# Kernel optimization log

Measured on AMD Instinct MI355X. Metric: run time of the kernel, lower is better.

Reference implementation:

```python
import jax, jax.numpy as jnp
import numpy as np

V, D, H, E, C, K = 16000, 1024, 1024, 8, 16, 2  # vocab, embed, expert hidden, n_experts, classes, top_k
B, S = 64, 512
GATE_H = 256


def setup_inputs() -> dict:
    key = jax.random.key(0)
    ks = jax.random.split(key, 11)
    s = lambda i, shape: jax.random.normal(ks[i], shape, jnp.float32) * 0.02
    return dict(
        x=jax.random.randint(ks[0], (B, S), 0, V),
        emb=s(1, (V, D)),                      # shared gating embedding
        gate_w1=s(2, (D, GATE_H)), gate_b1=jnp.zeros((GATE_H,), jnp.float32),
        gate_w2=s(3, (GATE_H, E)), gate_b2=jnp.zeros((E,), jnp.float32),
        exp_emb=s(4, (E, V, D)),               # per-expert embedding tables
        exp_w1=s(5, (E, D, H)), exp_b1=jnp.zeros((E, H), jnp.float32),
        exp_w2=s(6, (E, H, C)), exp_b2=jnp.zeros((E, C), jnp.float32),
    )


def reference(x, emb, gate_w1, gate_b1, gate_w2, gate_b2,
              exp_emb, exp_w1, exp_b1, exp_w2, exp_b2):
    # --- gating: embed, mean-pool over seq, 2-layer MLP, softmax, top-k ---
    pooled = emb[x].mean(axis=1)                                   # [B,D]
    logits = jax.nn.relu(pooled @ gate_w1 + gate_b1) @ gate_w2 + gate_b2  # [B,E]
    probs = jax.nn.softmax(logits, axis=-1)
    rw, idx = jax.lax.top_k(probs, K)                              # [B,K]
    rw = rw / rw.sum(axis=-1, keepdims=True)                       # renormalize

    # --- dispatch: gather each sample's assigned expert params (no per-sample loop) ---
    out = jnp.zeros((x.shape[0], C), jnp.float32)
    for k in range(K):  # tiny fixed loop over top_k
        e = idx[:, k]                                              # [B]
        tok = exp_emb[e[:, None], x]                               # [B,S,D]
        h = jax.nn.relu(jnp.einsum('bsd,bdh->bsh', tok, exp_w1[e]) + exp_b1[e][:, None, :])  # [B,S,H]
        p = h.mean(axis=1)                                         # [B,H]
        eo = jnp.einsum('bh,bhc->bc', p, exp_w2[e]) + exp_b2[e]    # [B,C]
        out = out + rw[:, k:k + 1] * eo
    return out
```

## Files before the change

### kernel.cpp

```cpp
#include <hip/hip_runtime.h>
#include <hip/hip_bf16.h>

#define V_   16000
#define D_   1024
#define H_   1024
#define E_   8
#define C_   16
#define B_   64
#define S_   512
#define GH_  256
#define NPAIR 128

typedef short  bf16x8 __attribute__((ext_vector_type(8)));
typedef ushort u16x8  __attribute__((ext_vector_type(8)));
typedef float  f32x4  __attribute__((ext_vector_type(4)));

static __device__ __forceinline__ ushort f2bf(float f) {
  union { float f; unsigned u; } un; un.f = f;
  unsigned u = un.u;
  return (ushort)((u + 0x7FFFu + ((u >> 16) & 1u)) >> 16);
}

static __device__ __forceinline__ unsigned pk2(float lo, float hi) {
  __hip_bfloat162 h = __float22bfloat162_rn(make_float2(lo, hi));
  unsigned r; __builtin_memcpy(&r, &h, sizeof(r)); return r;
}

__global__ void prep_kernel(const float* __restrict__ w1, ushort* __restrict__ w1t,
                            const int* __restrict__ x, const float* __restrict__ emb,
                            float* __restrict__ partial) {
  __shared__ float tile[64][65];
  const int id = blockIdx.x;
  if (id < 2048) {
    const int e = id >> 8, rem = id & 255;
    const int dtile = rem & 15, htile = rem >> 4;
    const int d0 = dtile * 64, h0 = htile * 64;
    const float* src = w1 + (size_t)e * D_ * H_;
    for (int i = threadIdx.x; i < 64 * 64; i += 256) {
      int r = i >> 6, c = i & 63;
      tile[r][c] = src[(size_t)(d0 + r) * H_ + h0 + c];
    }
    __syncthreads();
    for (int i = threadIdx.x; i < 512; i += 256) {
      int chunk = i >> 6, lane = i & 63;
      int kkl = chunk >> 2, htl = chunk & 3;
      int l15 = lane & 15, l16 = lane >> 4;
      u16x8 v;
      #pragma unroll
      for (int j = 0; j < 8; ++j)
        v[j] = f2bf(tile[kkl * 32 + l16 * 8 + j][htl * 16 + l15]);
      size_t off = ((size_t)((e * 32 + dtile * 2 + kkl) * 64 + htile * 4 + htl)) * 512 + lane * 8;
      *reinterpret_cast<u16x8*>(w1t + off) = v;
    }
  } else {
    const int pid = id - 2048;
    const int b = pid >> 3, sb = pid & 7, t = threadIdx.x;
    const int* xr = x + b * S_ + sb * 64;
    float4 acc = make_float4(0.f, 0.f, 0.f, 0.f);
    #pragma unroll 4
    for (int s = 0; s < 64; ++s) {
      const float4* row = reinterpret_cast<const float4*>(emb + (size_t)xr[s] * D_);
      float4 v = row[t];
      acc.x += v.x; acc.y += v.y; acc.z += v.z; acc.w += v.w;
    }
    reinterpret_cast<float4*>(partial + ((size_t)b * 8 + sb) * D_)[t] = acc;
  }
}

__global__ void gate_kernel(const float* __restrict__ partial,
                            const float* __restrict__ gw1, const float* __restrict__ gb1,
                            const float* __restrict__ gw2, const float* __restrict__ gb2,
                            int* __restrict__ ridx, float* __restrict__ rwgt) {
  const int b = blockIdx.x, j = threadIdx.x;
  __shared__ float pl[D_];
  __shared__ float hid[GH_];
  __shared__ float logits[E_];
  for (int d = j; d < D_; d += 256) {
    float s = 0.f;
    #pragma unroll
    for (int sb = 0; sb < 8; ++sb) s += partial[((size_t)b * 8 + sb) * D_ + d];
    pl[d] = s * (1.f / (float)S_);
  }
  __syncthreads();
  float acc = gb1[j];
  for (int d = 0; d < D_; ++d) acc += pl[d] * gw1[d * GH_ + j];
  hid[j] = fmaxf(acc, 0.f);
  __syncthreads();
  if (j < E_) {
    float l = gb2[j];
    for (int i = 0; i < GH_; ++i) l += hid[i] * gw2[i * E_ + j];
    logits[j] = l;
  }
  __syncthreads();
  if (j == 0) {
    int i0 = 0; float v0 = logits[0];
    for (int i = 1; i < E_; ++i) if (logits[i] > v0) { v0 = logits[i]; i0 = i; }
    int i1 = -1; float v1 = -3.0e38f;
    for (int i = 0; i < E_; ++i) {
      if (i == i0) continue;
      if (logits[i] > v1) { v1 = logits[i]; i1 = i; }
    }
    float r1 = expf(v1 - v0);
    float norm = 1.f + r1;
    ridx[b * 2 + 0] = i0;         ridx[b * 2 + 1] = i1;
    rwgt[b * 2 + 0] = 1.f / norm; rwgt[b * 2 + 1] = r1 / norm;
  }
}

__global__ void sort_pairs_kernel(const int* __restrict__ ridx, int* __restrict__ order) {
  __shared__ int se[NPAIR];
  const int t = threadIdx.x;
  se[t] = ridx[t];
  __syncthreads();
  const int e = se[t];
  int rank = 0;
  for (int j = 0; j < NPAIR; ++j) {
    const int ej = se[j];
    rank += (ej < e || (ej == e && j < t)) ? 1 : 0;
  }
  order[rank] = t;
}

__global__ __launch_bounds__(1024) void expert_kernel(
    const int* __restrict__ x, const float* __restrict__ exp_emb,
    const ushort* __restrict__ w1t, const float* __restrict__ exp_b1,
    const int* __restrict__ ridx, const int* __restrict__ order,
    float* __restrict__ p_part) {
  const int id     = blockIdx.x;
  const int xcd    = id & 7;
  const int within = id >> 3;
  const int slot   = xcd * 128 + within;
  const int pr     = order[slot >> 3];
  const int sblk   = slot & 7;
  const int b      = pr >> 1;
  const int tid    = threadIdx.x;

  __shared__ __align__(16) ushort lB[64 * 1024];

  const int e = ridx[pr];

  const int grow = tid >> 4, kq4 = (tid & 15) * 4;
  const int tok  = x[b * S_ + sblk * 64 + grow];
  const float* gptr = exp_emb + ((size_t)e * V_ + tok) * D_ + kq4;
  const int swz  = (grow & 7) << 3;
  const int gdst = grow * 1024 + (((kq4 & ~7) ^ swz) + (kq4 & 7));

  const int wid = tid >> 6, lane = tid & 63;
  const int l15 = lane & 15, l16 = lane >> 4;
  const int sw  = (l15 & 7) << 3;

  const ushort* aLane = w1t + (size_t)e * (32 * 64 * 512)
                        + ((size_t)wid * 4) * 512 + (size_t)lane * 8;
  #define LOADA(kk_, i_) \
    (*reinterpret_cast<const bf16x8*>(aLane + ((size_t)((kk_) * 64 + (i_))) * 512))

  f32x4 acc[4][4];
  #pragma unroll
  for (int i = 0; i < 4; ++i)
    #pragma unroll
    for (int j = 0; j < 4; ++j) acc[i][j] = (f32x4){0.f, 0.f, 0.f, 0.f};

  f32x4 stP[2];
  stP[0] = __builtin_nontemporal_load(reinterpret_cast<const f32x4*>(gptr));
  {
    uint2 w;
    w.x = pk2(stP[0][0], stP[0][1]); w.y = pk2(stP[0][2], stP[0][3]);
    *reinterpret_cast<uint2*>(&lB[gdst]) = w;
  }
  stP[1] = __builtin_nontemporal_load(reinterpret_cast<const f32x4*>(gptr + 64));
  __syncthreads();

  #pragma unroll
  for (int s = 0; s < 16; ++s) {
    const int cur = s & 1;
    if (s + 2 < 16) {
      stP[cur] = __builtin_nontemporal_load(
          reinterpret_cast<const f32x4*>(gptr + (s + 2) * 64));
    }
    #pragma unroll
    for (int ks = 0; ks < 2; ++ks) {
      const int kk = s * 2 + ks;
      const int colk = s * 64 + (((ks << 5) | (l16 << 3)) ^ sw);
      bf16x8 bfr[4], af[4];
      #pragma unroll
      for (int j = 0; j < 4; ++j)
        bfr[j] = *reinterpret_cast<const bf16x8*>(&lB[(j * 16 + l15) * 1024 + colk]);
      #pragma unroll
      for (int i = 0; i < 4; ++i) af[i] = LOADA(kk, i);
      #pragma unroll
      for (int i = 0; i < 4; ++i)
        #pragma unroll
        for (int j = 0; j < 4; ++j)
          acc[i][j] = __builtin_amdgcn_mfma_f32_16x16x32_bf16(af[i], bfr[j], acc[i][j], 0, 0, 0);
    }
    if (s + 1 < 16) {
      uint2 w;
      w.x = pk2(stP[cur ^ 1][0], stP[cur ^ 1][1]);
      w.y = pk2(stP[cur ^ 1][2], stP[cur ^ 1][3]);
      *reinterpret_cast<uint2*>(&lB[gdst + (s + 1) * 64]) = w;
    }
    __syncthreads();
  }
  #undef LOADA

  float* outRow = p_part + (size_t)(sblk * NPAIR + pr) * H_;
  const float* biasE = exp_b1 + e * H_;
  #pragma unroll
  for (int i = 0; i < 4; ++i) {
    #pragma unroll
    for (int r = 0; r < 4; ++r) {
      const int h = wid * 64 + i * 16 + l16 * 4 + r;
      const float bias = biasE[h];
      float v = 0.f;
      #pragma unroll
      for (int j = 0; j < 4; ++j) v += fmaxf(acc[i][j][r] + bias, 0.f);
      #pragma unroll
      for (int m = 1; m < 16; m <<= 1) v += __shfl_xor(v, m);
      if (l15 == 0) outRow[h] = v;
    }
  }
}

__global__ void finalize_kernel(const float* __restrict__ p_part,
                                const int* __restrict__ ridx, const float* __restrict__ rwgt,
                                const float* __restrict__ w2, const float* __restrict__ b2,
                                float* __restrict__ out) {
  const int b = blockIdx.x, t = threadIdx.x;
  const int c = t & 15, g = t >> 4;
  __shared__ float red[16][17];
  float res = 0.f;
  for (int kk = 0; kk < 2; ++kk) {
    const int pr = b * 2 + kk;
    const int e = ridx[pr];
    const float w = rwgt[pr];
    float dot = 0.f;
    for (int h = g; h < H_; h += 16) {
      float pm = 0.f;
      #pragma unroll
      for (int sb = 0; sb < 8; ++sb) pm += p_part[(size_t)(sb * NPAIR + pr) * H_ + h];
      dot += pm * w2[((size_t)e * H_ + h) * C_ + c];
    }
    red[g][c] = dot;
    __syncthreads();
    if (g == 0) {
      float s = 0.f;
      #pragma unroll
      for (int i = 0; i < 16; ++i) s += red[i][c];
      res += w * (s * (1.f / (float)S_) + b2[e * C_ + c]);
    }
    __syncthreads();
  }
  if (g == 0) out[b * C_ + c] = res;
}

extern "C" void kernel_launch(void* const* d_in, const int* in_sizes, int n_in,
                              void* d_out, int out_size, void* d_ws, size_t ws_size,
                              hipStream_t stream) {
  const int*   x    = (const int*)  d_in[0];
  const float* emb  = (const float*)d_in[1];
  const float* gw1  = (const float*)d_in[2];
  const float* gb1  = (const float*)d_in[3];
  const float* gw2  = (const float*)d_in[4];
  const float* gb2  = (const float*)d_in[5];
  const float* eemb = (const float*)d_in[6];
  const float* ew1  = (const float*)d_in[7];
  const float* eb1  = (const float*)d_in[8];
  const float* ew2  = (const float*)d_in[9];
  const float* eb2  = (const float*)d_in[10];
  float* out = (float*)d_out;

  char* ws = (char*)d_ws;
  const size_t OFF_W1T   = 0;
  const size_t OFF_PART  = (size_t)16 << 20;
  const size_t OFF_RIDX  = OFF_PART + ((size_t)2 << 20);
  const size_t OFF_RWGT  = OFF_RIDX + 1024;
  const size_t OFF_ORDER = OFF_RWGT + 1024;
  const size_t OFF_PPART = OFF_ORDER + 1024;

  ushort* w1t    = (ushort*)(ws + OFF_W1T);
  float*  part   = (float*) (ws + OFF_PART);
  int*    ridx   = (int*)   (ws + OFF_RIDX);
  float*  rwgt   = (float*) (ws + OFF_RWGT);
  int*    order  = (int*)   (ws + OFF_ORDER);
  float*  ppart  = (float*) (ws + OFF_PPART);

  prep_kernel<<<dim3(2560), 256, 0, stream>>>(ew1, w1t, x, emb, part);
  gate_kernel<<<dim3(B_), 256, 0, stream>>>(part, gw1, gb1, gw2, gb2, ridx, rwgt);
  sort_pairs_kernel<<<dim3(1), 128, 0, stream>>>(ridx, order);
  expert_kernel<<<dim3(1024), 1024, 0, stream>>>(x, eemb, w1t, eb1, ridx, order, ppart);
  finalize_kernel<<<dim3(B_), 256, 0, stream>>>(ppart, ridx, rwgt, ew2, eb2, out);
}
```

Baseline: 256.7 us.

## Retile expert GEMM to 128-token by 512-hidden blocks with double-buffered LDS

Each expert block now covers 128 tokens and half of the hidden dimension instead of 64 tokens and all of it. Each wave computes an 8x2 MFMA tile, so one A-fragment global load is reused across two B fragments. LDS shrinks from a full 64x1024 token tile to two 128x64 ping-pong buffers, so the gathered embeddings are staged per k-step instead of kept whole. This is meant to cut LDS footprint and per-block W1 traffic, at the cost of more partial sums (16 instead of 8) for finalize to reduce. Launch bounds now request 4 blocks per CU.

```diff
diff --git a/kernel.cpp b/kernel.cpp
--- a/kernel.cpp
+++ b/kernel.cpp
@@ -24,6 +24,13 @@
 static __device__ __forceinline__ unsigned pk2(float lo, float hi) {
   __hip_bfloat162 h = __float22bfloat162_rn(make_float2(lo, hi));
   unsigned r; __builtin_memcpy(&r, &h, sizeof(r)); return r;
+}
+
+static __device__ __forceinline__ uint4 cvt8(f32x4 a, f32x4 b) {
+  uint4 w;
+  w.x = pk2(a[0], a[1]); w.y = pk2(a[2], a[3]);
+  w.z = pk2(b[0], b[1]); w.w = pk2(b[2], b[3]);
+  return w;
 }
 
 __global__ void prep_kernel(const float* __restrict__ w1, ushort* __restrict__ w1t,
@@ -121,7 +128,7 @@
   order[rank] = t;
 }
 
-__global__ __launch_bounds__(1024) void expert_kernel(
+__global__ __launch_bounds__(1024, 4) void expert_kernel(
     const int* __restrict__ x, const float* __restrict__ exp_emb,
     const ushort* __restrict__ w1t, const float* __restrict__ exp_b1,
     const int* __restrict__ ridx, const int* __restrict__ order,
@@ -130,93 +137,95 @@
   const int xcd    = id & 7;
   const int within = id >> 3;
   const int slot   = xcd * 128 + within;
-  const int pr     = order[slot >> 3];
-  const int sblk   = slot & 7;
+  const int ss     = slot >> 3;
+  const int sb4    = (slot >> 1) & 3;
+  const int hb     = slot & 1;
+  const int pr     = order[ss];
   const int b      = pr >> 1;
   const int tid    = threadIdx.x;
 
-  __shared__ __align__(16) ushort lB[64 * 1024];
+  __shared__ __align__(16) ushort lB[2][8192];
 
   const int e = ridx[pr];
 
-  const int grow = tid >> 4, kq4 = (tid & 15) * 4;
-  const int tok  = x[b * S_ + sblk * 64 + grow];
-  const float* gptr = exp_emb + ((size_t)e * V_ + tok) * D_ + kq4;
-  const int swz  = (grow & 7) << 3;
-  const int gdst = grow * 1024 + (((kq4 & ~7) ^ swz) + (kq4 & 7));
+  const int grow = tid >> 3, gkq = (tid & 7) * 8;
+  const int tok  = x[b * S_ + sb4 * 128 + grow];
+  const float* gptr = exp_emb + ((size_t)e * V_ + tok) * D_ + gkq;
+  const int bwidx = grow * 64 + (gkq ^ ((grow & 7) << 3));
 
   const int wid = tid >> 6, lane = tid & 63;
   const int l15 = lane & 15, l16 = lane >> 4;
-  const int sw  = (l15 & 7) << 3;
+  const int ws = wid & 3, wh = wid >> 2;
+  const int sw = (l15 & 7) << 3;
 
   const ushort* aLane = w1t + (size_t)e * (32 * 64 * 512)
-                        + ((size_t)wid * 4) * 512 + (size_t)lane * 8;
+                        + ((size_t)(hb * 32 + wh * 8)) * 512 + (size_t)lane * 8;
   #define LOADA(kk_, i_) \
     (*reinterpret_cast<const bf16x8*>(aLane + ((size_t)((kk_) * 64 + (i_))) * 512))
 
-  f32x4 acc[4][4];
+  f32x4 acc[8][2];
   #pragma unroll
-  for (int i = 0; i < 4; ++i)
+  for (int i = 0; i < 8; ++i)
     #pragma unroll
-    for (int j = 0; j < 4; ++j) acc[i][j] = (f32x4){0.f, 0.f, 0.f, 0.f};
-
-  f32x4 stP[2];
-  stP[0] = __builtin_nontemporal_load(reinterpret_cast<const f32x4*>(gptr));
-  {
-    uint2 w;
-    w.x = pk2(stP[0][0], stP[0][1]); w.y = pk2(stP[0][2], stP[0][3]);
-    *reinterpret_cast<uint2*>(&lB[gdst]) = w;
-  }
-  stP[1] = __builtin_nontemporal_load(reinterpret_cast<const f32x4*>(gptr + 64));
+    for (int j = 0; j < 2; ++j) acc[i][j] = (f32x4){0.f, 0.f, 0.f, 0.f};
+
+  f32x4 stP[2][2];
+  stP[0][0] = __builtin_nontemporal_load(reinterpret_cast<const f32x4*>(gptr));
+  stP[0][1] = __builtin_nontemporal_load(reinterpret_cast<const f32x4*>(gptr + 4));
+  *reinterpret_cast<uint4*>(&lB[0][bwidx]) = cvt8(stP[0][0], stP[0][1]);
+  stP[1][0] = __builtin_nontemporal_load(reinterpret_cast<const f32x4*>(gptr + 64));
+  stP[1][1] = __builtin_nontemporal_load(reinterpret_cast<const f32x4*>(gptr + 68));
   __syncthreads();
 
   #pragma unroll
   for (int s = 0; s < 16; ++s) {
     const int cur = s & 1;
     if (s + 2 < 16) {
-      stP[cur] = __builtin_nontemporal_load(
+      stP[cur][0] = __builtin_nontemporal_load(
           reinterpret_cast<const f32x4*>(gptr + (s + 2) * 64));
+      stP[cur][1] = __builtin_nontemporal_load(
+          reinterpret_cast<const f32x4*>(gptr + (s + 2) * 64 + 4));
     }
     #pragma unroll
     for (int ks = 0; ks < 2; ++ks) {
       const int kk = s * 2 + ks;
-      const int colk = s * 64 + (((ks << 5) | (l16 << 3)) ^ sw);
-      bf16x8 bfr[4], af[4];
-      #pragma unroll
-      for (int j = 0; j < 4; ++j)
-        bfr[j] = *reinterpret_cast<const bf16x8*>(&lB[(j * 16 + l15) * 1024 + colk]);
-      #pragma unroll
-      for (int i = 0; i < 4; ++i) af[i] = LOADA(kk, i);
-      #pragma unroll
-      for (int i = 0; i < 4; ++i)
+      const int colk = ((ks << 5) | (l16 << 3)) ^ sw;
+      bf16x8 bfr[2];
+      #pragma unroll
+      for (int j = 0; j < 2; ++j) {
+        const int row = ws * 32 + j * 16 + l15;
+        bfr[j] = *reinterpret_cast<const bf16x8*>(
+            &lB[cur][row * 64 + (((ks << 5) | (l16 << 3)) ^ ((row & 7) << 3))]);
+      }
+      #pragma unroll
+      for (int i = 0; i < 8; ++i) {
+        const bf16x8 af = LOADA(kk, i);
         #pragma unroll
-        for (int j = 0; j < 4; ++j)
-          acc[i][j] = __builtin_amdgcn_mfma_f32_16x16x32_bf16(af[i], bfr[j], acc[i][j], 0, 0, 0);
+        for (int j = 0; j < 2; ++j)
+          acc[i][j] = __builtin_amdgcn_mfma_f32_16x16x32_bf16(af, bfr[j], acc[i][j], 0, 0, 0);
+      }
+      (void)colk;
     }
     if (s + 1 < 16) {
-      uint2 w;
-      w.x = pk2(stP[cur ^ 1][0], stP[cur ^ 1][1]);
-      w.y = pk2(stP[cur ^ 1][2], stP[cur ^ 1][3]);
-      *reinterpret_cast<uint2*>(&lB[gdst + (s + 1) * 64]) = w;
+      *reinterpret_cast<uint4*>(&lB[cur ^ 1][bwidx]) =
+          cvt8(stP[cur ^ 1][0], stP[cur ^ 1][1]);
     }
     __syncthreads();
   }
   #undef LOADA
 
-  float* outRow = p_part + (size_t)(sblk * NPAIR + pr) * H_;
-  const float* biasE = exp_b1 + e * H_;
+  float* outRow = p_part + (size_t)((sb4 * 4 + ws) * NPAIR + pr) * H_ + hb * 512 + wh * 128;
+  const float* biasE = exp_b1 + e * H_ + hb * 512 + wh * 128;
   #pragma unroll
-  for (int i = 0; i < 4; ++i) {
+  for (int i = 0; i < 8; ++i) {
     #pragma unroll
     for (int r = 0; r < 4; ++r) {
-      const int h = wid * 64 + i * 16 + l16 * 4 + r;
-      const float bias = biasE[h];
-      float v = 0.f;
-      #pragma unroll
-      for (int j = 0; j < 4; ++j) v += fmaxf(acc[i][j][r] + bias, 0.f);
+      const int hl = i * 16 + l16 * 4 + r;
+      const float bias = biasE[hl];
+      float v = fmaxf(acc[i][0][r] + bias, 0.f) + fmaxf(acc[i][1][r] + bias, 0.f);
       #pragma unroll
       for (int m = 1; m < 16; m <<= 1) v += __shfl_xor(v, m);
-      if (l15 == 0) outRow[h] = v;
+      if (l15 == 0) outRow[hl] = v;
     }
   }
 }
@@ -237,7 +246,7 @@
     for (int h = g; h < H_; h += 16) {
       float pm = 0.f;
       #pragma unroll
-      for (int sb = 0; sb < 8; ++sb) pm += p_part[(size_t)(sb * NPAIR + pr) * H_ + h];
+      for (int sb = 0; sb < 16; ++sb) pm += p_part[(size_t)(sb * NPAIR + pr) * H_ + h];
       dot += pm * w2[((size_t)e * H_ + h) * C_ + c];
     }
     red[g][c] = dot;
```

New measurement: 368.8 us. +43.7%, slower.

## Retile expert GEMM to 256 tokens x 256 hidden blocks with double-buffered LDS

Applied to the files above, without the earlier changes.

Each expert block now covers 256 tokens and a quarter of the hidden dimension instead of 64 tokens and the full hidden dimension. Each wave works on a 64-token by 64-hidden subtile. The staged embedding tile is cut to 64-wide K slices in a double-buffered LDS array, which shrinks LDS use and lets more blocks stay resident (launch_bounds min-blocks set to 4). This also changes the reuse balance: each w1 fragment loaded from global memory now feeds more tokens, while each gathered embedding row is read by four hidden blocks. The partial-output layout grows to 4x more slices per sblk, and finalize has to sum them correctly. That part is not visible, so it is a risk.

```diff
diff --git a/kernel.cpp b/kernel.cpp
--- a/kernel.cpp
+++ b/kernel.cpp
@@ -24,6 +24,13 @@
 static __device__ __forceinline__ unsigned pk2(float lo, float hi) {
   __hip_bfloat162 h = __float22bfloat162_rn(make_float2(lo, hi));
   unsigned r; __builtin_memcpy(&r, &h, sizeof(r)); return r;
+}
+
+static __device__ __forceinline__ uint4 cvt8(f32x4 a, f32x4 b) {
+  uint4 w;
+  w.x = pk2(a[0], a[1]); w.y = pk2(a[2], a[3]);
+  w.z = pk2(b[0], b[1]); w.w = pk2(b[2], b[3]);
+  return w;
 }
 
 __global__ void prep_kernel(const float* __restrict__ w1, ushort* __restrict__ w1t,
@@ -121,7 +128,7 @@
   order[rank] = t;
 }
 
-__global__ __launch_bounds__(1024) void expert_kernel(
+__global__ __launch_bounds__(1024, 4) void expert_kernel(
     const int* __restrict__ x, const float* __restrict__ exp_emb,
     const ushort* __restrict__ w1t, const float* __restrict__ exp_b1,
     const int* __restrict__ ridx, const int* __restrict__ order,
@@ -130,27 +137,32 @@
   const int xcd    = id & 7;
   const int within = id >> 3;
   const int slot   = xcd * 128 + within;
-  const int pr     = order[slot >> 3];
-  const int sblk   = slot & 7;
+  const int ss     = slot >> 3;
+  const int sub    = slot & 7;
+  const int sblk   = sub >> 2;
+  const int hblk   = sub & 3;
+  const int pr     = order[ss];
   const int b      = pr >> 1;
   const int tid    = threadIdx.x;
 
-  __shared__ __align__(16) ushort lB[64 * 1024];
+  __shared__ __align__(16) ushort lB[2][16384];
 
   const int e = ridx[pr];
 
-  const int grow = tid >> 4, kq4 = (tid & 15) * 4;
-  const int tok  = x[b * S_ + sblk * 64 + grow];
-  const float* gptr = exp_emb + ((size_t)e * V_ + tok) * D_ + kq4;
-  const int swz  = (grow & 7) << 3;
-  const int gdst = grow * 1024 + (((kq4 & ~7) ^ swz) + (kq4 & 7));
+  const int grow = tid >> 2, q = tid & 3;
+  const int tok  = x[b * S_ + sblk * 256 + grow];
+  const float* gptr = exp_emb + ((size_t)e * V_ + tok) * D_ + q * 16;
+  const int swr = (grow & 7) << 3;
+  const int bw0 = grow * 64 + ((q * 16) ^ swr);
+  const int bw1 = grow * 64 + ((q * 16 + 8) ^ swr);
 
   const int wid = tid >> 6, lane = tid & 63;
   const int l15 = lane & 15, l16 = lane >> 4;
-  const int sw  = (l15 & 7) << 3;
+  const int ws = wid & 3, wh = wid >> 2;
+  const int sw = (l15 & 7) << 3;
 
   const ushort* aLane = w1t + (size_t)e * (32 * 64 * 512)
-                        + ((size_t)wid * 4) * 512 + (size_t)lane * 8;
+                        + ((size_t)(hblk * 16 + wh * 4)) * 512 + (size_t)lane * 8;
   #define LOADA(kk_, i_) \
     (*reinterpret_cast<const bf16x8*>(aLane + ((size_t)((kk_) * 64 + (i_))) * 512))
 
@@ -160,31 +172,37 @@
     #pragma unroll
     for (int j = 0; j < 4; ++j) acc[i][j] = (f32x4){0.f, 0.f, 0.f, 0.f};
 
-  f32x4 stP[2];
-  stP[0] = __builtin_nontemporal_load(reinterpret_cast<const f32x4*>(gptr));
-  {
-    uint2 w;
-    w.x = pk2(stP[0][0], stP[0][1]); w.y = pk2(stP[0][2], stP[0][3]);
-    *reinterpret_cast<uint2*>(&lB[gdst]) = w;
-  }
-  stP[1] = __builtin_nontemporal_load(reinterpret_cast<const f32x4*>(gptr + 64));
+  f32x4 stP[2][4];
+  #pragma unroll
+  for (int t4 = 0; t4 < 4; ++t4)
+    stP[0][t4] = __builtin_nontemporal_load(reinterpret_cast<const f32x4*>(gptr + t4 * 4));
+  *reinterpret_cast<uint4*>(&lB[0][bw0]) = cvt8(stP[0][0], stP[0][1]);
+  *reinterpret_cast<uint4*>(&lB[0][bw1]) = cvt8(stP[0][2], stP[0][3]);
+  #pragma unroll
+  for (int t4 = 0; t4 < 4; ++t4)
+    stP[1][t4] = __builtin_nontemporal_load(reinterpret_cast<const f32x4*>(gptr + 64 + t4 * 4));
   __syncthreads();
 
   #pragma unroll
   for (int s = 0; s < 16; ++s) {
     const int cur = s & 1;
     if (s + 2 < 16) {
-      stP[cur] = __builtin_nontemporal_load(
-          reinterpret_cast<const f32x4*>(gptr + (s + 2) * 64));
+      #pragma unroll
+      for (int t4 = 0; t4 < 4; ++t4)
+        stP[cur][t4] = __builtin_nontemporal_load(
+            reinterpret_cast<const f32x4*>(gptr + (s + 2) * 64 + t4 * 4));
     }
     #pragma unroll
     for (int ks = 0; ks < 2; ++ks) {
       const int kk = s * 2 + ks;
-      const int colk = s * 64 + (((ks << 5) | (l16 << 3)) ^ sw);
+      const int colk = ((ks << 5) | (l16 << 3));
       bf16x8 bfr[4], af[4];
       #pragma unroll
-      for (int j = 0; j < 4; ++j)
-        bfr[j] = *reinterpret_cast<const bf16x8*>(&lB[(j * 16 + l15) * 1024 + colk]);
+      for (int j = 0; j < 4; ++j) {
+        const int row = ws * 64 + j * 16 + l15;
+        bfr[j] = *reinterpret_cast<const bf16x8*>(
+            &lB[cur][row * 64 + (colk ^ ((row & 7) << 3))]);
+      }
       #pragma unroll
       for (int i = 0; i < 4; ++i) af[i] = LOADA(kk, i);
       #pragma unroll
@@ -194,29 +212,28 @@
           acc[i][j] = __builtin_amdgcn_mfma_f32_16x16x32_bf16(af[i], bfr[j], acc[i][j], 0, 0, 0);
     }
     if (s + 1 < 16) {
-      uint2 w;
-      w.x = pk2(stP[cur ^ 1][0], stP[cur ^ 1][1]);
-      w.y = pk2(stP[cur ^ 1][2], stP[cur ^ 1][3]);
-      *reinterpret_cast<uint2*>(&lB[gdst + (s + 1) * 64]) = w;
+      *reinterpret_cast<uint4*>(&lB[cur ^ 1][bw0]) = cvt8(stP[cur ^ 1][0], stP[cur ^ 1][1]);
+      *reinterpret_cast<uint4*>(&lB[cur ^ 1][bw1]) = cvt8(stP[cur ^ 1][2], stP[cur ^ 1][3]);
     }
     __syncthreads();
   }
   #undef LOADA
 
-  float* outRow = p_part + (size_t)(sblk * NPAIR + pr) * H_;
-  const float* biasE = exp_b1 + e * H_;
+  float* outRow = p_part + (size_t)((sblk * 4 + ws) * NPAIR + pr) * H_
+                  + hblk * 256 + wh * 64;
+  const float* biasE = exp_b1 + e * H_ + hblk * 256 + wh * 64;
   #pragma unroll
   for (int i = 0; i < 4; ++i) {
     #pragma unroll
     for (int r = 0; r < 4; ++r) {
-      const int h = wid * 64 + i * 16 + l16 * 4 + r;
-      const float bias = biasE[h];
+      const int hl = i * 16 + l16 * 4 + r;
+      const float bias = biasE[hl];
       float v = 0.f;
       #pragma unroll
       for (int j = 0; j < 4; ++j) v += fmaxf(acc[i][j][r] + bias, 0.f);
       #pragma unroll
       for (int m = 1; m < 16; m <<= 1) v += __shfl_xor(v, m);
-      if (l15 == 0) outRow[h] = v;
+      if (l15 == 0) outRow[hl] = v;
     }
   }
 }
```

New measurement: 445.4 us. 73.5% more time.
